# Kernel tuning notes

Hardware: AMD Instinct MI355X
Metric: run time of the kernel (lower is better)

Reference implementation:

```python
import jax, jax.numpy as jnp
import numpy as np

T, N = 32, 256
HID, NL = 64, 1
D_CH, Hg, Wg = 2, 8, 8            # obs shape (2, 8, 8); d must be 2 to match Conv2d(2*HID, 2*HID)
NSUB, SUBDIM = 6, 3               # subtasks shape (n_subtasks, subtask_dim)
OBS_V, SUB_V, NACT = 16, 20, 6    # vocab sizes; action_space.n = NSUB
OBS_LEN = D_CH * Hg * Wg          # 128
SUB_LEN = NSUB * SUBDIM           # 18
GRU_IN = HID * (OBS_LEN + SUBDIM) # 8384
STATE = 2 + NL * HID + NACT + NSUB  # a(1)+v(1)+h(64)+a_probs(6)+p(6) = 78


def setup_inputs() -> dict:
    key = jax.random.key(0)
    ks = jax.random.split(key, 12)
    obs_idx = jax.random.randint(ks[0], (T, N, OBS_LEN), 0, OBS_V)
    sub_idx = jax.random.randint(ks[1], (T, N, SUB_LEN), 0, SUB_V)
    act = jax.random.randint(ks[2], (T, N, 1), 0, NACT)  # all >= 0 -> sample_new is a no-op
    inputs = jnp.concatenate([obs_idx, sub_idx, act], -1).astype(jnp.float32)
    hx = jnp.zeros((1, N, STATE), jnp.float32)  # all-zero -> new_episode everywhere
    sd = lambda f: 1.0 / np.sqrt(f)
    return dict(
        inputs=inputs,
        hx=hx,
        subtask_emb=jax.random.normal(ks[3], (SUB_V, HID)),
        obs_emb=jax.random.normal(ks[4], (OBS_V, HID)),
        conv_w=jax.random.normal(ks[5], (2 * HID, 2 * HID)) * sd(2 * HID),
        conv_b=jnp.zeros((2 * HID,)),
        w_ih=jax.random.normal(ks[6], (3 * HID, GRU_IN)) * sd(GRU_IN),
        w_hh=jax.random.normal(ks[7], (3 * HID, HID)) * sd(HID),
        b_ih=jnp.zeros((3 * HID,)),
        b_hh=jnp.zeros((3 * HID,)),
        critic_w=jax.random.normal(ks[8], (1, HID)) * sd(HID),
        critic_b=jnp.zeros((1,)),
        phi_w=jax.random.normal(ks[9], (1, HID)) * sd(HID),
        phi_b=jnp.zeros((1,)),
    )


def _forward(inputs, hx, subtask_emb, obs_emb, conv_w, conv_b, w_ih, w_hh,
             b_ih, b_hh, critic_w, critic_b, phi_w, phi_b):
    ints = inputs.astype(jnp.int32)
    obs_all = ints[:, :, :OBS_LEN]                      # (T,N,128)
    sub_all = ints[:, :, OBS_LEN:OBS_LEN + SUB_LEN]     # (T,N,18)
    act_all = ints[:, :, -1]                            # (T,N)

    # subtask memory from first timestep: (N, NSUB, SUBDIM*HID)
    M = subtask_emb[sub_all[0]].reshape(N, NSUB, SUBDIM * HID)

    hx0 = hx[0]
    new_episode = jnp.all(hx0 == 0, axis=-1)            # (N,)
    # recurrent state split order a(1), v(1), h(NL*HID), a_probs(NACT), p(NSUB)
    h0 = hx0[:, 2:2 + NL * HID].reshape(N, NL, HID).transpose(1, 0, 2)  # (NL,N,HID)
    p0 = hx0[:, 2 + NL * HID + NACT:]
    p0 = p0.at[:, 0].set(jnp.where(new_episode, 1.0, p0[:, 0]))

    def gru_cell(x, h):
        gx = x @ w_ih.T + b_ih
        gh = h @ w_hh.T + b_hh
        r = jax.nn.sigmoid(gx[:, :HID] + gh[:, :HID])
        z = jax.nn.sigmoid(gx[:, HID:2 * HID] + gh[:, HID:2 * HID])
        n = jnp.tanh(gx[:, 2 * HID:] + r * gh[:, 2 * HID:])
        return (1 - z) * n + z * h

    def step(carry, xt):
        h, p = carry
        obs_t, act_t = xt
        r_vec = jnp.einsum('ns,nsk->nk', p, M)          # (p.unsqueeze(1) @ M).squeeze(1)
        emb = obs_emb[obs_t.reshape(N, D_CH, Hg, Wg)]   # (N,2,H,W,HID)
        conv_in = emb.transpose(0, 1, 4, 2, 3).reshape(N, 2 * HID, Hg * Wg)
        conv_out = jnp.einsum('ncp,oc->nop', conv_in, conv_w) + conv_b[None, :, None]  # 1x1 conv
        gru_in = jnp.concatenate([conv_out.reshape(N, -1), r_vec], -1)
        hn = gru_cell(gru_in, h[0])                     # single-layer GRU, seq len 1
        h_new = hn[None]
        c = jax.nn.sigmoid(hn @ phi_w.T + phi_b)        # (N,1)
        # torch.roll(F.pad(p,(0,1)), 1) flattened: pad column is 0, so this is a
        # right-shift with 0 fill; p1[:, -1] == p[:, -1].
        p1 = jnp.concatenate([jnp.zeros((N, 1), p.dtype), p[:, :-1]], axis=1)
        p2 = p1 + p * p[:, -1:]
        p_new = (1 - c) * p + c * p2
        probs = p_new / p_new.sum(-1, keepdims=True)    # FixedCategorical(p).probs
        v = hn @ critic_w.T + critic_b                  # (N,1)
        a = act_t.astype(jnp.float32)[:, None]          # actions all >=0 -> no resampling
        h_flat = h_new.transpose(1, 0, 2).reshape(N, -1)
        ys = jnp.concatenate([a, v, h_flat, probs, p_new], -1)
        return (h_new, p_new), ys

    _, hx_out = jax.lax.scan(step, (h0, p0), (obs_all, act_all))  # (T,N,78)
    return hx_out


def reference(inputs, hx, subtask_emb, obs_emb, conv_w, conv_b, w_ih, w_hh,
              b_ih, b_hh, critic_w, critic_b, phi_w, phi_b):
    hx_out = _forward(inputs, hx, subtask_emb, obs_emb, conv_w, conv_b, w_ih,
                      w_hh, b_ih, b_hh, critic_w, critic_b, phi_w, phi_b)
    return (hx_out, hx_out[-1:])
```

## Files before the change

### kernel.cpp

```cpp
#include <hip/hip_runtime.h>
#include <hip/hip_bf16.h>
#include <math.h>

#define TT 32
#define NN 256
#define HID 64
#define OBS_LEN 128
#define SUB_LEN 18
#define IN_ROW 147
#define GJ 192
#define GRU_IN 8384
#define STATE 78
#define NSUB 6
#define NT_TILES 1572

__device__ __forceinline__ float sigm(float x) {
    return 1.0f / (1.0f + __expf(-x));
}

__device__ __forceinline__ unsigned short f2bf(float f) {
    unsigned u = __float_as_uint(f);
    u += 0x7fffu + ((u >> 16) & 1u);
    return (unsigned short)(u >> 16);
}

__device__ __forceinline__ float2 pkfma(float2 a, float2 b, float2 c) {
    float2 r;
    r.x = fmaf(a.x, b.x, c.x);
    r.y = fmaf(a.y, b.y, c.y);
    return r;
}

__global__ __launch_bounds__(256) void k_TGC(const float* __restrict__ w_ih,
                                             const float* __restrict__ obs_emb,
                                             const float* __restrict__ conv_w,
                                             const float* __restrict__ conv_b,
                                             const float* __restrict__ b_ih,
                                             float* __restrict__ wT,
                                             float* __restrict__ G,
                                             float* __restrict__ CB2) {
    int b = blockIdx.x;
    int tid = threadIdx.x;
    __shared__ float tile[32][33];
    __shared__ float red[4];

    if (b < NT_TILES) {
        int bx = b % 262, by = b / 262;
        int i0 = bx * 32, j0 = by * 32;
        int tx = tid & 31, ty = tid >> 5;
        for (int a = ty; a < 32; a += 8)
            tile[a][tx] = w_ih[(size_t)(j0 + a) * GRU_IN + i0 + tx];
        __syncthreads();
        for (int a = ty; a < 32; a += 8)
            wT[(size_t)(i0 + a) * GJ + j0 + tx] = tile[tx][a];
    } else if (b < NT_TILES + 16) {
        int i = (b - NT_TILES) * 256 + tid;
        int v = i & 15, d = (i >> 4) & 1, o = i >> 5;
        float acc = 0.f;
        const float* oe = obs_emb + v * 64;
        const float* cw = conv_w + o * 128 + d * 64;
        #pragma unroll
        for (int hd = 0; hd < 64; hd++) acc = fmaf(oe[hd], cw[hd], acc);
        G[i] = acc;
    } else {
        int j = b - (NT_TILES + 16);
        const float* wr = w_ih + (size_t)j * GRU_IN;
        float acc = 0.f;
        for (int i = tid; i < 8192; i += 256) acc = fmaf(conv_b[i >> 6], wr[i], acc);
        for (int off = 32; off > 0; off >>= 1) acc += __shfl_down(acc, off, 64);
        if ((tid & 63) == 0) red[tid >> 6] = acc;
        __syncthreads();
        if (tid == 0) CB2[j] = b_ih[j] + red[0] + red[1] + red[2] + red[3];
    }
}

__global__ __launch_bounds__(192) void k_EQ(const float* __restrict__ inputs,
                                            const float* __restrict__ subtask_emb,
                                            const float* __restrict__ G,
                                            const float* __restrict__ wT,
                                            unsigned short* __restrict__ E16,
                                            float* __restrict__ Q) {
    int b = blockIdx.x;
    int j = threadIdx.x;

    if (b < 256) {
        int dp = b >> 1, half = b & 1;
        int d = dp >> 6, p = dp & 63;
        __shared__ __align__(16) float Gs[128 * 8];
        for (int e = j; e < 1024; e += GJ) {
            int o = e >> 3, vv = e & 7;
            Gs[e] = G[(o << 5) + (d << 4) + (half << 3) + vv];
        }
        __syncthreads();
        float acc[8];
        #pragma unroll
        for (int v = 0; v < 8; v++) acc[v] = 0.f;
        const float* wb = wT + (size_t)p * GJ + j;
        #pragma unroll 4
        for (int o = 0; o < 128; o++) {
            float w = wb[(size_t)(o * 64) * GJ];
            float4 g0 = *(const float4*)&Gs[o * 8];
            float4 g1 = *(const float4*)&Gs[o * 8 + 4];
            acc[0] = fmaf(g0.x, w, acc[0]);
            acc[1] = fmaf(g0.y, w, acc[1]);
            acc[2] = fmaf(g0.z, w, acc[2]);
            acc[3] = fmaf(g0.w, w, acc[3]);
            acc[4] = fmaf(g1.x, w, acc[4]);
            acc[5] = fmaf(g1.y, w, acc[5]);
            acc[6] = fmaf(g1.z, w, acc[6]);
            acc[7] = fmaf(g1.w, w, acc[7]);
        }
        unsigned short* Eo = E16 + ((size_t)(dp * 16 + half * 8)) * GJ;
        #pragma unroll
        for (int v = 0; v < 8; v++) Eo[v * GJ + j] = f2bf(acc[v]);
    } else {
        int n = b - 256;
        __shared__ int sidx[SUB_LEN];
        __shared__ __align__(16) float Ms[GJ * 8];
        if (j < SUB_LEN) sidx[j] = (int)inputs[(size_t)n * IN_ROW + OBS_LEN + j];
        __syncthreads();
        for (int e = j; e < NSUB * GJ; e += GJ) {
            int s = e / GJ, k = e - s * GJ;
            int row = sidx[s * 3 + (k >> 6)];
            Ms[k * 8 + s] = subtask_emb[row * 64 + (k & 63)];
        }
        __syncthreads();
        float acc[NSUB] = {0.f, 0.f, 0.f, 0.f, 0.f, 0.f};
        const float* base = wT + (size_t)8192 * GJ + j;
        #pragma unroll 4
        for (int k = 0; k < GJ; k++) {
            float w = base[(size_t)k * GJ];
            float4 m0 = *(const float4*)&Ms[k * 8];
            float2 m1 = *(const float2*)&Ms[k * 8 + 4];
            acc[0] = fmaf(m0.x, w, acc[0]);
            acc[1] = fmaf(m0.y, w, acc[1]);
            acc[2] = fmaf(m0.z, w, acc[2]);
            acc[3] = fmaf(m0.w, w, acc[3]);
            acc[4] = fmaf(m1.x, w, acc[4]);
            acc[5] = fmaf(m1.y, w, acc[5]);
        }
        for (int s = 0; s < NSUB; s++) Q[((size_t)n * NSUB + s) * GJ + j] = acc[s];
    }
}

__global__ __launch_bounds__(192) void k_gx(const float* __restrict__ inputs,
                                            const unsigned short* __restrict__ E16,
                                            const float* __restrict__ CB2,
                                            float* __restrict__ gx_all) {
    int tn0 = blockIdx.x * 2;
    int tid = threadIdx.x;
    int g = tid / 96;
    int jj = (tid - g * 96) * 2;
    int tn = tn0 + g;
    __shared__ int idx[2][OBS_LEN];
    for (int e = tid; e < 2 * OBS_LEN; e += 192)
        idx[e >> 7][e & 127] = (int)inputs[(size_t)(tn0 + (e >> 7)) * IN_ROW + (e & 127)];
    __syncthreads();
    float a0 = CB2[jj], a1 = CB2[jj + 1];
    const int* id = idx[g];
    #pragma unroll 8
    for (int dp = 0; dp < OBS_LEN; dp++) {
        unsigned u = *(const unsigned*)(E16 + ((size_t)(dp * 16 + id[dp])) * GJ + jj);
        a0 += __uint_as_float(u << 16);
        a1 += __uint_as_float(u & 0xffff0000u);
    }
    float2 r; r.x = a0; r.y = a1;
    *(float2*)(gx_all + (size_t)tn * GJ + jj) = r;
}

__global__ __launch_bounds__(64, 1) void k_rec(const float* __restrict__ inputs,
                                               const float* __restrict__ hx,
                                               const float* __restrict__ w_hh,
                                               const float* __restrict__ b_hh,
                                               const float* __restrict__ critic_w,
                                               const float* __restrict__ critic_b,
                                               const float* __restrict__ phi_w,
                                               const float* __restrict__ phi_b,
                                               const float* __restrict__ Q,
                                               const float* __restrict__ gx_all,
                                               float* __restrict__ out) {
    int n = blockIdx.x;
    int lane = threadIdx.x;

    __shared__ __align__(16) float gx_lds[TT * GJ];
    __shared__ __align__(16) float h_sh[64];
    __shared__ float act_sh[TT];

    for (int e = lane * 4; e < TT * GJ; e += 64 * 4) {
        int t = e / GJ, j = e - t * GJ;
        *(float4*)&gx_lds[e] = *(const float4*)(gx_all + ((size_t)t * NN + n) * GJ + j);
    }
    if (lane < TT)
        act_sh[lane] = inputs[((size_t)lane * NN + n) * IN_ROW + (IN_ROW - 1)];

    float2 w0[32], w1[32], w2[32];
    {
        const float4* r0 = (const float4*)(w_hh + (size_t)lane * 64);
        const float4* r1 = (const float4*)(w_hh + (size_t)(64 + lane) * 64);
        const float4* r2 = (const float4*)(w_hh + (size_t)(128 + lane) * 64);
        #pragma unroll
        for (int h4 = 0; h4 < 16; h4++) {
            float4 a = r0[h4]; w0[2*h4] = make_float2(a.x, a.y); w0[2*h4+1] = make_float2(a.z, a.w);
            float4 c = r1[h4]; w1[2*h4] = make_float2(c.x, c.y); w1[2*h4+1] = make_float2(c.z, c.w);
            float4 d = r2[h4]; w2[2*h4] = make_float2(d.x, d.y); w2[2*h4+1] = make_float2(d.z, d.w);
        }
    }
    float q0[NSUB], q1[NSUB], q2[NSUB];
    #pragma unroll
    for (int s = 0; s < NSUB; s++) {
        const float* qb = Q + ((size_t)n * NSUB + s) * GJ;
        q0[s] = qb[lane]; q1[s] = qb[64 + lane]; q2[s] = qb[128 + lane];
    }
    float bh0 = b_hh[lane], bh1 = b_hh[64 + lane], bh2 = b_hh[128 + lane];
    float pw = phi_w[lane], cw = critic_w[lane];
    float phib = phi_b[0], crtb = critic_b[0];

    float v0 = hx[(size_t)n * STATE + lane];
    float v1 = (lane < STATE - 64) ? hx[(size_t)n * STATE + 64 + lane] : 0.f;
    unsigned long long bal0 = __ballot(v0 != 0.f);
    unsigned long long bal1 = __ballot((lane < STATE - 64) && v1 != 0.f);
    bool ne = ((bal0 | bal1) == 0ULL);
    float h_own = hx[(size_t)n * STATE + 2 + lane];
    float p0, p1, p2, p3, p4, p5;
    {
        const float* pb = hx + (size_t)n * STATE + 72;
        p0 = pb[0]; p1 = pb[1]; p2 = pb[2]; p3 = pb[3]; p4 = pb[4]; p5 = pb[5];
    }
    if (ne) p0 = 1.0f;
    h_sh[lane] = h_own;

    for (int t = 0; t < TT; t++) {
        float gx0 = gx_lds[t * GJ + lane];
        float gx1 = gx_lds[t * GJ + 64 + lane];
        float gx2 = gx_lds[t * GJ + 128 + lane];
        gx0 = fmaf(p0, q0[0], gx0); gx1 = fmaf(p0, q1[0], gx1); gx2 = fmaf(p0, q2[0], gx2);
        gx0 = fmaf(p1, q0[1], gx0); gx1 = fmaf(p1, q1[1], gx1); gx2 = fmaf(p1, q2[1], gx2);
        gx0 = fmaf(p2, q0[2], gx0); gx1 = fmaf(p2, q1[2], gx1); gx2 = fmaf(p2, q2[2], gx2);
        gx0 = fmaf(p3, q0[3], gx0); gx1 = fmaf(p3, q1[3], gx1); gx2 = fmaf(p3, q2[3], gx2);
        gx0 = fmaf(p4, q0[4], gx0); gx1 = fmaf(p4, q1[4], gx1); gx2 = fmaf(p4, q2[4], gx2);
        gx0 = fmaf(p5, q0[5], gx0); gx1 = fmaf(p5, q1[5], gx1); gx2 = fmaf(p5, q2[5], gx2);
        float2 a0 = make_float2(0.f, 0.f), a1 = a0, a2 = a0;
        #pragma unroll
        for (int h4 = 0; h4 < 16; h4++) {
            float4 hh = *(const float4*)&h_sh[h4 * 4];
            float2 hA = make_float2(hh.x, hh.y);
            float2 hB = make_float2(hh.z, hh.w);
            a0 = pkfma(hA, w0[2*h4], a0); a0 = pkfma(hB, w0[2*h4+1], a0);
            a1 = pkfma(hA, w1[2*h4], a1); a1 = pkfma(hB, w1[2*h4+1], a1);
            a2 = pkfma(hA, w2[2*h4], a2); a2 = pkfma(hB, w2[2*h4+1], a2);
        }
        float gh0 = bh0 + a0.x + a0.y;
        float gh1 = bh1 + a1.x + a1.y;
        float gh2 = bh2 + a2.x + a2.y;

        float r = sigm(gx0 + gh0);
        float z = sigm(gx1 + gh1);
        float x2 = fmaf(r, gh2, gx2);
        float e2 = __expf(2.f * x2);
        float nv = 1.f - 2.f / (e2 + 1.f);
        float hn = fmaf(z, h_own - nv, nv);

        float pc = hn * pw, vc = hn * cw;
        #pragma unroll
        for (int off = 32; off > 0; off >>= 1) {
            pc += __shfl_xor(pc, off, 64);
            vc += __shfl_xor(vc, off, 64);
        }
        float c = sigm(pc + phib);
        float v = vc + crtb;

        float n0 = fmaf(c, (p0 * p5)      - p0, p0);
        float n1 = fmaf(c, (p0 + p1 * p5) - p1, p1);
        float n2 = fmaf(c, (p1 + p2 * p5) - p2, p2);
        float n3 = fmaf(c, (p2 + p3 * p5) - p3, p3);
        float n4 = fmaf(c, (p3 + p4 * p5) - p4, p4);
        float n5 = fmaf(c, (p4 + p5 * p5) - p5, p5);
        float psum = ((n0 + n1) + (n2 + n3)) + (n4 + n5);
        float rinv = 1.0f / psum;

        size_t base = ((size_t)t * NN + n) * STATE;
        out[base + 2 + lane] = hn;
        int sidx = (lane < 6) ? lane : lane - 6;
        float ppick = n0;
        ppick = (sidx == 1) ? n1 : ppick;
        ppick = (sidx == 2) ? n2 : ppick;
        ppick = (sidx == 3) ? n3 : ppick;
        ppick = (sidx == 4) ? n4 : ppick;
        ppick = (sidx == 5) ? n5 : ppick;
        if (lane < 12) {
            out[base + 66 + lane] = (lane < 6) ? ppick * rinv : ppick;
        } else if (lane < 14) {
            out[base + (lane - 12)] = (lane == 12) ? act_sh[t] : v;
        }
        if (t == TT - 1) {
            size_t b2 = (size_t)TT * NN * STATE + (size_t)n * STATE;
            out[b2 + 2 + lane] = hn;
            if (lane < 12) out[b2 + 66 + lane] = (lane < 6) ? ppick * rinv : ppick;
            else if (lane < 14) out[b2 + (lane - 12)] = (lane == 12) ? act_sh[t] : v;
        }

        h_sh[lane] = hn;
        h_own = hn;
        p0 = n0; p1 = n1; p2 = n2; p3 = n3; p4 = n4; p5 = n5;
    }
}

extern "C" void kernel_launch(void* const* d_in, const int* in_sizes, int n_in,
                              void* d_out, int out_size, void* d_ws, size_t ws_size,
                              hipStream_t stream) {
    const float* inputs      = (const float*)d_in[0];
    const float* hx          = (const float*)d_in[1];
    const float* subtask_emb = (const float*)d_in[2];
    const float* obs_emb     = (const float*)d_in[3];
    const float* conv_w      = (const float*)d_in[4];
    const float* conv_b      = (const float*)d_in[5];
    const float* w_ih        = (const float*)d_in[6];
    const float* w_hh        = (const float*)d_in[7];
    const float* b_ih        = (const float*)d_in[8];
    const float* b_hh        = (const float*)d_in[9];
    const float* critic_w    = (const float*)d_in[10];
    const float* critic_b    = (const float*)d_in[11];
    const float* phi_w       = (const float*)d_in[12];
    const float* phi_b       = (const float*)d_in[13];
    float* out = (float*)d_out;

    float* ws   = (float*)d_ws;
    float* wT   = ws;
    float* G    = wT + (size_t)GRU_IN * GJ;
    float* CB2  = G + 4096;
    float* Ef   = CB2 + 192;
    unsigned short* E16 = (unsigned short*)Ef;
    float* Q    = Ef + 196608;
    float* gx   = Q + (size_t)NN * NSUB * GJ;

    k_TGC<<<NT_TILES + 16 + GJ, 256, 0, stream>>>(w_ih, obs_emb, conv_w, conv_b,
                                                  b_ih, wT, G, CB2);
    k_EQ<<<512, GJ, 0, stream>>>(inputs, subtask_emb, G, wT, E16, Q);
    k_gx<<<TT * NN / 2, GJ, 0, stream>>>(inputs, E16, CB2, gx);
    k_rec<<<NN, 64, 0, stream>>>(inputs, hx, w_hh, b_hh, critic_w, critic_b,
                                 phi_w, phi_b, Q, gx, out);
}
```

Before: 188.9 us.

## Use fp16 dot2 in GRU recurrence and defer phi reduction to next step

```diff
diff --git a/kernel.cpp b/kernel.cpp
--- a/kernel.cpp
+++ b/kernel.cpp
@@ -14,6 +14,8 @@
 #define NSUB 6
 #define NT_TILES 1572
 
+typedef __fp16 half2_t __attribute__((ext_vector_type(2)));
+
 __device__ __forceinline__ float sigm(float x) {
     return 1.0f / (1.0f + __expf(-x));
 }
@@ -24,11 +26,18 @@
     return (unsigned short)(u >> 16);
 }
 
-__device__ __forceinline__ float2 pkfma(float2 a, float2 b, float2 c) {
-    float2 r;
-    r.x = fmaf(a.x, b.x, c.x);
-    r.y = fmaf(a.y, b.y, c.y);
-    return r;
+#if defined(__has_builtin)
+#if __has_builtin(__builtin_amdgcn_fdot2)
+#define HAVE_FDOT2 1
+#endif
+#endif
+
+__device__ __forceinline__ float fdot2(half2_t a, half2_t b, float c) {
+#ifdef HAVE_FDOT2
+    return __builtin_amdgcn_fdot2(a, b, c, false);
+#else
+    return fmaf((float)a.x, (float)b.x, fmaf((float)a.y, (float)b.y, c));
+#endif
 }
 
 __global__ __launch_bounds__(256) void k_TGC(const float* __restrict__ w_ih,
@@ -48,11 +57,13 @@
         int bx = b % 262, by = b / 262;
         int i0 = bx * 32, j0 = by * 32;
         int tx = tid & 31, ty = tid >> 5;
-        for (int a = ty; a < 32; a += 8)
-            tile[a][tx] = w_ih[(size_t)(j0 + a) * GRU_IN + i0 + tx];
+        #pragma unroll
+        for (int a = 0; a < 4; a++)
+            tile[ty + a * 8][tx] = w_ih[(size_t)(j0 + ty + a * 8) * GRU_IN + i0 + tx];
         __syncthreads();
-        for (int a = ty; a < 32; a += 8)
-            wT[(size_t)(i0 + a) * GJ + j0 + tx] = tile[tx][a];
+        #pragma unroll
+        for (int a = 0; a < 4; a++)
+            wT[(size_t)(i0 + ty + a * 8) * GJ + j0 + tx] = tile[tx][ty + a * 8];
     } else if (b < NT_TILES + 16) {
         int i = (b - NT_TILES) * 256 + tid;
         int v = i & 15, d = (i >> 4) & 1, o = i >> 5;
@@ -66,6 +77,7 @@
         int j = b - (NT_TILES + 16);
         const float* wr = w_ih + (size_t)j * GRU_IN;
         float acc = 0.f;
+        #pragma unroll 8
         for (int i = tid; i < 8192; i += 256) acc = fmaf(conv_b[i >> 6], wr[i], acc);
         for (int off = 32; off > 0; off >>= 1) acc += __shfl_down(acc, off, 64);
         if ((tid & 63) == 0) red[tid >> 6] = acc;
@@ -96,7 +108,7 @@
         #pragma unroll
         for (int v = 0; v < 8; v++) acc[v] = 0.f;
         const float* wb = wT + (size_t)p * GJ + j;
-        #pragma unroll 4
+        #pragma unroll 8
         for (int o = 0; o < 128; o++) {
             float w = wb[(size_t)(o * 64) * GJ];
             float4 g0 = *(const float4*)&Gs[o * 8];
@@ -127,7 +139,7 @@
         __syncthreads();
         float acc[NSUB] = {0.f, 0.f, 0.f, 0.f, 0.f, 0.f};
         const float* base = wT + (size_t)8192 * GJ + j;
-        #pragma unroll 4
+        #pragma unroll 8
         for (int k = 0; k < GJ; k++) {
             float w = base[(size_t)k * GJ];
             float4 m0 = *(const float4*)&Ms[k * 8];
@@ -147,25 +159,28 @@
                                             const unsigned short* __restrict__ E16,
                                             const float* __restrict__ CB2,
                                             float* __restrict__ gx_all) {
-    int tn0 = blockIdx.x * 2;
+    int tn0 = blockIdx.x * 4;
     int tid = threadIdx.x;
-    int g = tid / 96;
-    int jj = (tid - g * 96) * 2;
-    int tn = tn0 + g;
-    __shared__ int idx[2][OBS_LEN];
-    for (int e = tid; e < 2 * OBS_LEN; e += 192)
+    __shared__ int idx[4][OBS_LEN];
+    for (int e = tid; e < 4 * OBS_LEN; e += 192)
         idx[e >> 7][e & 127] = (int)inputs[(size_t)(tn0 + (e >> 7)) * IN_ROW + (e & 127)];
     __syncthreads();
-    float a0 = CB2[jj], a1 = CB2[jj + 1];
-    const int* id = idx[g];
-    #pragma unroll 8
+    int r = tid / 48, l = tid - r * 48;
+    int jj = l * 4;
+    int tn = tn0 + r;
+    float4 cb = *(const float4*)(CB2 + jj);
+    float a0 = cb.x, a1 = cb.y, a2 = cb.z, a3 = cb.w;
+    const int* id = idx[r];
+    #pragma unroll 16
     for (int dp = 0; dp < OBS_LEN; dp++) {
-        unsigned u = *(const unsigned*)(E16 + ((size_t)(dp * 16 + id[dp])) * GJ + jj);
-        a0 += __uint_as_float(u << 16);
-        a1 += __uint_as_float(u & 0xffff0000u);
-    }
-    float2 r; r.x = a0; r.y = a1;
-    *(float2*)(gx_all + (size_t)tn * GJ + jj) = r;
+        uint2 u = *(const uint2*)(E16 + ((size_t)(dp * 16 + id[dp])) * GJ + jj);
+        a0 += __uint_as_float(u.x << 16);
+        a1 += __uint_as_float(u.x & 0xffff0000u);
+        a2 += __uint_as_float(u.y << 16);
+        a3 += __uint_as_float(u.y & 0xffff0000u);
+    }
+    float4 o4; o4.x = a0; o4.y = a1; o4.z = a2; o4.w = a3;
+    *(float4*)(gx_all + (size_t)tn * GJ + jj) = o4;
 }
 
 __global__ __launch_bounds__(64, 1) void k_rec(const float* __restrict__ inputs,
@@ -183,7 +198,7 @@
     int lane = threadIdx.x;
 
     __shared__ __align__(16) float gx_lds[TT * GJ];
-    __shared__ __align__(16) float h_sh[64];
+    __shared__ __align__(16) __fp16 h16[64];
     __shared__ float act_sh[TT];
 
     for (int e = lane * 4; e < TT * GJ; e += 64 * 4) {
@@ -193,16 +208,32 @@
     if (lane < TT)
         act_sh[lane] = inputs[((size_t)lane * NN + n) * IN_ROW + (IN_ROW - 1)];
 
-    float2 w0[32], w1[32], w2[32];
+    half2_t wv0[32], wv1[32], wv2[32];
     {
         const float4* r0 = (const float4*)(w_hh + (size_t)lane * 64);
         const float4* r1 = (const float4*)(w_hh + (size_t)(64 + lane) * 64);
         const float4* r2 = (const float4*)(w_hh + (size_t)(128 + lane) * 64);
         #pragma unroll
         for (int h4 = 0; h4 < 16; h4++) {
-            float4 a = r0[h4]; w0[2*h4] = make_float2(a.x, a.y); w0[2*h4+1] = make_float2(a.z, a.w);
-            float4 c = r1[h4]; w1[2*h4] = make_float2(c.x, c.y); w1[2*h4+1] = make_float2(c.z, c.w);
-            float4 d = r2[h4]; w2[2*h4] = make_float2(d.x, d.y); w2[2*h4+1] = make_float2(d.z, d.w);
+            float4 a = r0[h4];
+            wv0[2*h4]   = __builtin_amdgcn_cvt_pkrtz(a.x, a.y);
+            wv0[2*h4+1] = __builtin_amdgcn_cvt_pkrtz(a.z, a.w);
+            float4 c = r1[h4];
+            wv1[2*h4]   = __builtin_amdgcn_cvt_pkrtz(c.x, c.y);
+            wv1[2*h4+1] = __builtin_amdgcn_cvt_pkrtz(c.z, c.w);
+            float4 d = r2[h4];
+            wv2[2*h4]   = __builtin_amdgcn_cvt_pkrtz(d.x, d.y);
+            wv2[2*h4+1] = __builtin_amdgcn_cvt_pkrtz(d.z, d.w);
+        }
+    }
+    half2_t ph[32];
+    {
+        const float4* pp = (const float4*)phi_w;
+        #pragma unroll
+        for (int h4 = 0; h4 < 16; h4++) {
+            float4 a = pp[h4];
+            ph[2*h4]   = __builtin_amdgcn_cvt_pkrtz(a.x, a.y);
+            ph[2*h4+1] = __builtin_amdgcn_cvt_pkrtz(a.z, a.w);
         }
     }
     float q0[NSUB], q1[NSUB], q2[NSUB];
@@ -212,7 +243,7 @@
         q0[s] = qb[lane]; q1[s] = qb[64 + lane]; q2[s] = qb[128 + lane];
     }
     float bh0 = b_hh[lane], bh1 = b_hh[64 + lane], bh2 = b_hh[128 + lane];
-    float pw = phi_w[lane], cw = critic_w[lane];
+    float cw_own = critic_w[lane];
     float phib = phi_b[0], crtb = critic_b[0];
 
     float v0 = hx[(size_t)n * STATE + lane];
@@ -227,9 +258,63 @@
         p0 = pb[0]; p1 = pb[1]; p2 = pb[2]; p3 = pb[3]; p4 = pb[4]; p5 = pb[5];
     }
     if (ne) p0 = 1.0f;
-    h_sh[lane] = h_own;
+    h16[lane] = (__fp16)h_own;
+
+    float vlast = 0.f;
+
+    auto finalize = [&](int tf, float pc) {
+        float c = sigm(pc + phib);
+        float n0 = fmaf(c, (p0 * p5)      - p0, p0);
+        float n1 = fmaf(c, (p0 + p1 * p5) - p1, p1);
+        float n2 = fmaf(c, (p1 + p2 * p5) - p2, p2);
+        float n3 = fmaf(c, (p2 + p3 * p5) - p3, p3);
+        float n4 = fmaf(c, (p3 + p4 * p5) - p4, p4);
+        float n5 = fmaf(c, (p4 + p5 * p5) - p5, p5);
+        float psum = ((n0 + n1) + (n2 + n3)) + (n4 + n5);
+        float rinv = 1.0f / psum;
+        if (lane < 12) {
+            int s = (lane < 6) ? lane : lane - 6;
+            float pp = n0;
+            pp = (s == 1) ? n1 : pp;
+            pp = (s == 2) ? n2 : pp;
+            pp = (s == 3) ? n3 : pp;
+            pp = (s == 4) ? n4 : pp;
+            pp = (s == 5) ? n5 : pp;
+            size_t fb = ((size_t)tf * NN + n) * STATE;
+            out[fb + ((lane < 6) ? (72 + lane) : (66 + lane - 6))] =
+                (lane < 6) ? pp : pp * rinv;
+        }
+        p0 = n0; p1 = n1; p2 = n2; p3 = n3; p4 = n4; p5 = n5;
+    };
 
     for (int t = 0; t < TT; t++) {
+        uint4 raw[8];
+        #pragma unroll
+        for (int rix = 0; rix < 8; rix++) raw[rix] = ((const uint4*)h16)[rix];
+        half2_t h2[32];
+        {
+            const unsigned* rw = (const unsigned*)raw;
+            #pragma unroll
+            for (int k = 0; k < 32; k++) h2[k] = __builtin_bit_cast(half2_t, rw[k]);
+        }
+
+        float A0 = 0.f, B0 = 0.f, A1 = 0.f, B1 = 0.f, A2 = 0.f, B2 = 0.f;
+        float PA = 0.f, PB = 0.f;
+        #pragma unroll
+        for (int k = 0; k < 16; k++) {
+            A0 = fdot2(h2[k], wv0[k], A0);
+            B0 = fdot2(h2[16 + k], wv0[16 + k], B0);
+            A1 = fdot2(h2[k], wv1[k], A1);
+            B1 = fdot2(h2[16 + k], wv1[16 + k], B1);
+            A2 = fdot2(h2[k], wv2[k], A2);
+            B2 = fdot2(h2[16 + k], wv2[16 + k], B2);
+            PA = fdot2(h2[k], ph[k], PA);
+            PB = fdot2(h2[16 + k], ph[16 + k], PB);
+        }
+        float pc = PA + PB;
+
+        if (t > 0) finalize(t - 1, pc);
+
         float gx0 = gx_lds[t * GJ + lane];
         float gx1 = gx_lds[t * GJ + 64 + lane];
         float gx2 = gx_lds[t * GJ + 128 + lane];
@@ -239,19 +324,10 @@
         gx0 = fmaf(p3, q0[3], gx0); gx1 = fmaf(p3, q1[3], gx1); gx2 = fmaf(p3, q2[3], gx2);
         gx0 = fmaf(p4, q0[4], gx0); gx1 = fmaf(p4, q1[4], gx1); gx2 = fmaf(p4, q2[4], gx2);
         gx0 = fmaf(p5, q0[5], gx0); gx1 = fmaf(p5, q1[5], gx1); gx2 = fmaf(p5, q2[5], gx2);
-        float2 a0 = make_float2(0.f, 0.f), a1 = a0, a2 = a0;
-        #pragma unroll
-        for (int h4 = 0; h4 < 16; h4++) {
-            float4 hh = *(const float4*)&h_sh[h4 * 4];
-            float2 hA = make_float2(hh.x, hh.y);
-            float2 hB = make_float2(hh.z, hh.w);
-            a0 = pkfma(hA, w0[2*h4], a0); a0 = pkfma(hB, w0[2*h4+1], a0);
-            a1 = pkfma(hA, w1[2*h4], a1); a1 = pkfma(hB, w1[2*h4+1], a1);
-            a2 = pkfma(hA, w2[2*h4], a2); a2 = pkfma(hB, w2[2*h4+1], a2);
-        }
-        float gh0 = bh0 + a0.x + a0.y;
-        float gh1 = bh1 + a1.x + a1.y;
-        float gh2 = bh2 + a2.x + a2.y;
+
+        float gh0 = bh0 + A0 + B0;
+        float gh1 = bh1 + A1 + B1;
+        float gh2 = bh2 + A2 + B2;
 
         float r = sigm(gx0 + gh0);
         float z = sigm(gx1 + gh1);
@@ -260,48 +336,50 @@
         float nv = 1.f - 2.f / (e2 + 1.f);
         float hn = fmaf(z, h_own - nv, nv);
 
-        float pc = hn * pw, vc = hn * cw;
-        #pragma unroll
-        for (int off = 32; off > 0; off >>= 1) {
-            pc += __shfl_xor(pc, off, 64);
-            vc += __shfl_xor(vc, off, 64);
-        }
-        float c = sigm(pc + phib);
-        float v = vc + crtb;
-
-        float n0 = fmaf(c, (p0 * p5)      - p0, p0);
-        float n1 = fmaf(c, (p0 + p1 * p5) - p1, p1);
-        float n2 = fmaf(c, (p1 + p2 * p5) - p2, p2);
-        float n3 = fmaf(c, (p2 + p3 * p5) - p3, p3);
-        float n4 = fmaf(c, (p3 + p4 * p5) - p4, p4);
-        float n5 = fmaf(c, (p4 + p5 * p5) - p5, p5);
-        float psum = ((n0 + n1) + (n2 + n3)) + (n4 + n5);
-        float rinv = 1.0f / psum;
-
         size_t base = ((size_t)t * NN + n) * STATE;
         out[base + 2 + lane] = hn;
-        int sidx = (lane < 6) ? lane : lane - 6;
-        float ppick = n0;
-        ppick = (sidx == 1) ? n1 : ppick;
-        ppick = (sidx == 2) ? n2 : ppick;
-        ppick = (sidx == 3) ? n3 : ppick;
-        ppick = (sidx == 4) ? n4 : ppick;
-        ppick = (sidx == 5) ? n5 : ppick;
+        float vc = hn * cw_own;
+        #pragma unroll
+        for (int off = 32; off > 0; off >>= 1) vc += __shfl_xor(vc, off, 64);
+        vlast = vc + crtb;
+        if (lane == 0) out[base + 1] = vlast;
+        else if (lane == 1) out[base + 0] = act_sh[t];
+
+        h16[lane] = (__fp16)hn;
+        h_own = hn;
+    }
+
+    {
+        uint4 raw[8];
+        #pragma unroll
+        for (int rix = 0; rix < 8; rix++) raw[rix] = ((const uint4*)h16)[rix];
+        const unsigned* rw = (const unsigned*)raw;
+        float PA = 0.f, PB = 0.f;
+        #pragma unroll
+        for (int k = 0; k < 16; k++) {
+            PA = fdot2(__builtin_bit_cast(half2_t, rw[k]), ph[k], PA);
+            PB = fdot2(__builtin_bit_cast(half2_t, rw[16 + k]), ph[16 + k], PB);
+        }
+        finalize(TT - 1, PA + PB);
+        float psum = ((p0 + p1) + (p2 + p3)) + (p4 + p5);
+        float rinv = 1.0f / psum;
+        size_t fs = (size_t)TT * NN * STATE + (size_t)n * STATE;
+        out[fs + 2 + lane] = h_own;
         if (lane < 12) {
-            out[base + 66 + lane] = (lane < 6) ? ppick * rinv : ppick;
-        } else if (lane < 14) {
-            out[base + (lane - 12)] = (lane == 12) ? act_sh[t] : v;
-        }
-        if (t == TT - 1) {
-            size_t b2 = (size_t)TT * NN * STATE + (size_t)n * STATE;
-            out[b2 + 2 + lane] = hn;
-            if (lane < 12) out[b2 + 66 + lane] = (lane < 6) ? ppick * rinv : ppick;
-            else if (lane < 14) out[b2 + (lane - 12)] = (lane == 12) ? act_sh[t] : v;
-        }
-
-        h_sh[lane] = hn;
-        h_own = hn;
-        p0 = n0; p1 = n1; p2 = n2; p3 = n3; p4 = n4; p5 = n5;
+            int s = (lane < 6) ? lane : lane - 6;
+            float pp = p0;
+            pp = (s == 1) ? p1 : pp;
+            pp = (s == 2) ? p2 : pp;
+            pp = (s == 3) ? p3 : pp;
+            pp = (s == 4) ? p4 : pp;
+            pp = (s == 5) ? p5 : pp;
+            out[fs + ((lane < 6) ? (72 + lane) : (66 + lane - 6))] =
+                (lane < 6) ? pp : pp * rinv;
+        } else if (lane == 12) {
+            out[fs + 0] = act_sh[TT - 1];
+        } else if (lane == 13) {
+            out[fs + 1] = vlast;
+        }
     }
 }
 
@@ -336,7 +414,7 @@
     k_TGC<<<NT_TILES + 16 + GJ, 256, 0, stream>>>(w_ih, obs_emb, conv_w, conv_b,
                                                   b_ih, wT, G, CB2);
     k_EQ<<<512, GJ, 0, stream>>>(inputs, subtask_emb, G, wT, E16, Q);
-    k_gx<<<TT * NN / 2, GJ, 0, stream>>>(inputs, E16, CB2, gx);
+    k_gx<<<TT * NN / 4, GJ, 0, stream>>>(inputs, E16, CB2, gx);
     k_rec<<<NN, 64, 0, stream>>>(inputs, hx, w_hh, b_hh, critic_w, critic_b,
                                  phi_w, phi_b, Q, gx, out);
 }
```

Measured after the change: 178.3 us. 5.6% less time.
